# Kernel tuning notes

Measured on AMD Instinct MI355X. Metric: run time of the kernel, lower is better.

Reference implementation:

```python
import jax, jax.numpy as jnp
import numpy as np

VOCAB = 32000
DIM = 256
LAYERS = 2
CLASSES = 8
BATCH = 32
SEQ = 8192


def setup_inputs() -> dict:
    key = jax.random.key(0)
    ks = jax.random.split(key, 8)
    s = 1.0 / np.sqrt(DIM)
    x = jax.random.randint(ks[0], (BATCH, SEQ), 0, VOCAB, dtype=jnp.int32)
    emb = jax.random.normal(ks[1], (VOCAB, DIM), dtype=jnp.float32)
    Wz = jax.random.normal(ks[2], (LAYERS, DIM, DIM), dtype=jnp.float32) * s
    bz = jnp.zeros((LAYERS, DIM), dtype=jnp.float32)
    Wh = jax.random.normal(ks[3], (LAYERS, DIM, DIM), dtype=jnp.float32) * s
    bh = jnp.zeros((LAYERS, DIM), dtype=jnp.float32)
    Wo = jax.random.normal(ks[4], (DIM, CLASSES), dtype=jnp.float32) * s
    bo = jnp.zeros((CLASSES,), dtype=jnp.float32)
    return {"x": x, "emb": emb, "Wz": Wz, "bz": bz, "Wh": Wh, "bh": bh, "Wo": Wo, "bo": bo}


def _min_gru_layer(h_in, Wz_l, bz_l, Wh_l, bh_l):
    # minGRU: z_t = sigmoid(W_z x_t); h~_t = W_h x_t
    # h_t = (1 - z_t) * h_{t-1} + z_t * h~_t,  h_0 = 0
    z = jax.nn.sigmoid(jnp.einsum('bsd,de->bse', h_in, Wz_l) + bz_l)
    h_tilde = jnp.einsum('bsd,de->bse', h_in, Wh_l) + bh_l
    a = 1.0 - z          # decay coefficient
    b = z * h_tilde      # input contribution
    # parallel associative scan of h_t = a_t * h_{t-1} + b_t (h_0 = 0)
    def combine(c1, c2):
        a1, b1 = c1
        a2, b2 = c2
        return a1 * a2, b1 * a2 + b2
    _, h = jax.lax.associative_scan(combine, (a, b), axis=1)
    return h


def reference(x, emb, Wz, bz, Wh, bh, Wo, bo):
    h = emb[x]  # [B, S, D]
    for l in range(LAYERS):
        h = _min_gru_layer(h, Wz[l], bz[l], Wh[l], bh[l])
    # classifier on the last timestep
    return h[:, -1] @ Wo + bo  # [B, CLASSES]
```

## Files before the change

kernel.cpp:

```cpp
#include <hip/hip_runtime.h>
#include <stdint.h>

#define SEQ 8192
#define CS 64
#define NCH 128
#define NBLK 4096

typedef float f32x4 __attribute__((ext_vector_type(4)));
typedef short short8 __attribute__((ext_vector_type(8)));
typedef unsigned short u16;
typedef u16 ushort8 __attribute__((ext_vector_type(8)));
typedef u16 ushort4v __attribute__((ext_vector_type(4)));

__device__ __forceinline__ u16 f2bf(float f) {
  uint32_t u = __float_as_uint(f);
  u += 0x7fffu + ((u >> 16) & 1u);
  return (u16)(u >> 16);
}

__device__ __forceinline__ void gld16(void* lds, const void* g) {
  __builtin_amdgcn_global_load_lds(
      (const __attribute__((address_space(1))) uint32_t*)g,
      (__attribute__((address_space(3))) uint32_t*)lds, 16, 0, 0);
}

__global__ void embq_kernel(const float* __restrict__ emb, u16* __restrict__ embq) {
  int i = (blockIdx.x * 256 + threadIdx.x) * 4;
  float4 v = *(const float4*)(emb + i);
  ushort4v p;
  p[0] = f2bf(v.x); p[1] = f2bf(v.y); p[2] = f2bf(v.z); p[3] = f2bf(v.w);
  *(ushort4v*)(embq + i) = p;
}

__global__ void wt_kernel(const float* __restrict__ Wz, const float* __restrict__ Wh,
                          u16* __restrict__ WtS) {
  int idx = blockIdx.x * 256 + threadIdx.x;
  int d = idx & 255;
  int k = (idx >> 8) & 255;
  int m = idx >> 16;
  const float* src = (m < 2 ? Wz : Wh) + (size_t)(m & 1) * 65536;
  float v = src[k * 256 + d];
  int dh = d >> 6, dloc = d & 63, k32 = k >> 5, kl = k & 31;
  size_t tile = ((size_t)(m * 4 + dh) * 8 + k32) * 4096;
  size_t byte = (size_t)(dloc * 64 + ((kl * 2) ^ (((dloc >> 1) & 3) << 4)));
  *(u16*)((char*)WtS + tile + byte) = f2bf(v);
}

__device__ __forceinline__ void stage32(char* dst, const char* WtSb, int mat, int k32,
                                        int w, int lane) {
  const int dh = w >> 1, half = w & 1;
  const char* src = WtSb + ((size_t)((mat * 4 + dh) * 8 + k32)) * 4096 + half * 2048 + lane * 16;
  char* d = dst + dh * 4096 + half * 2048;
  gld16(d, src);
  gld16(d + 1024, src + 1024);
}

__device__ __forceinline__ void load_fa(const u16* As, int k32, int wr, int l15, int lg,
                                        short8 (&fa)[2]) {
  const int xm = (l15 & 7) << 4;
  const int kt = k32 >> 1, ks = k32 & 1;
  #pragma unroll
  for (int mi = 0; mi < 2; mi++)
    fa[mi] = *(const short8*)((const char*)As + kt * 8192 +
               (((wr * 32 + mi * 16 + l15) * 128 + ks * 64 + lg * 16) ^ xm));
}

__device__ __forceinline__ void mfma_frags(const char* P, const short8 (&fa)[2],
    int wc, int l15, int lg, f32x4 (&acc)[2][4])
{
  #pragma unroll
  for (int ni = 0; ni < 4; ni++) {
    const int dloc = ni * 16 + l15;
    const int off = dloc * 64 + ((lg * 16) ^ (((dloc >> 1) & 3) << 4));
    short8 fb = *(const short8*)(P + wc * 4096 + off);
    #pragma unroll
    for (int mi = 0; mi < 2; mi++)
      acc[mi][ni] = __builtin_amdgcn_mfma_f32_16x16x32_bf16(fa[mi], fb, acc[mi][ni], 0, 0, 0);
  }
}

__device__ __forceinline__ void gemm_pipe3(int lsel, const char* WtSb, const u16* As,
    char* Pb, int w, int wr, int wc, int l15, int lg, int lane,
    f32x4 (&accz)[2][4], f32x4 (&acch)[2][4])
{
  stage32(Pb,         WtSb, lsel,     0, w, lane);
  stage32(Pb + 16384, WtSb, 2 + lsel, 0, w, lane);
  short8 fa[2];
  #pragma unroll
  for (int i = 0; i < 16; ++i) {
    if (i < 15) asm volatile("s_waitcnt vmcnt(2)" ::: "memory");
    else        asm volatile("s_waitcnt vmcnt(0)" ::: "memory");
    __builtin_amdgcn_s_barrier();
    __builtin_amdgcn_sched_barrier(0);
    if (i + 2 < 16)
      stage32(Pb + ((i + 2) % 3) * 16384, WtSb,
              ((i + 2) & 1) ? (2 + lsel) : lsel, (i + 2) >> 1, w, lane);
    if ((i & 1) == 0) {
      load_fa(As, i >> 1, wr, l15, lg, fa);
      mfma_frags(Pb + (i % 3) * 16384, fa, wc, l15, lg, accz);
    } else {
      mfma_frags(Pb + (i % 3) * 16384, fa, wc, l15, lg, acch);
    }
  }
}

__device__ __forceinline__ float2* seg_ptr(char* segt, int s, int d) {
  return (float2*)(segt + s * 2048 + ((d * 8) ^ (s << 4)));
}

template<int PHASE>
__global__ __launch_bounds__(512, 4)
void gru_kernel(const int* __restrict__ x, const u16* __restrict__ embq,
                const u16* __restrict__ WtS,
                const float* __restrict__ bz0, const float* __restrict__ bh0,
                const float* __restrict__ bz1, const float* __restrict__ bh1,
                const float* __restrict__ carry,
                float* __restrict__ Ap, float* __restrict__ Bs)
{
  __shared__ __align__(16) u16 As[16384];
  __shared__ __align__(16) char Pb[49152];

  const int tid = threadIdx.x;
  const int lane = tid & 63;
  const int w = tid >> 6;
  const int wr = w >> 2, wc = w & 3;
  const int l15 = lane & 15, lg = lane >> 4;
  const int cb = blockIdx.x;
  const int b = cb >> 7, c = cb & (NCH - 1);
  const char* WtSb = (const char*)WtS;
  char* segt = (char*)As;

  {
    const int sm = tid >> 3, kq = tid & 7;
    const int tok = x[b * SEQ + c * CS + sm];
    const u16* src = embq + (size_t)tok * 256 + kq * 32;
    char* sub = (char*)As + (kq >> 1) * 8192;
    const int kb = (kq & 1) * 64;
    const int swz = (sm & 7) << 4;
    #pragma unroll
    for (int j = 0; j < 4; j++) {
      ushort8 p = *(const ushort8*)(src + j * 8);
      *(ushort8*)(sub + ((sm * 128 + kb + j * 16) ^ swz)) = p;
    }
  }

  f32x4 accz[2][4], acch[2][4];
  #pragma unroll
  for (int i = 0; i < 2; i++)
    #pragma unroll
    for (int j = 0; j < 4; j++) {
      f32x4 zz = {0.f, 0.f, 0.f, 0.f};
      accz[i][j] = zz; acch[i][j] = zz;
    }

  __syncthreads();
  gemm_pipe3(0, WtSb, As, Pb, w, wr, wc, l15, lg, lane, accz, acch);
  __syncthreads();

  #pragma unroll
  for (int ni = 0; ni < 4; ni++) {
    const int d = wc * 64 + ni * 16 + l15;
    const float bzv = bz0[d];
    const float bhv = bh0[d];
    #pragma unroll
    for (int mi = 0; mi < 2; mi++) {
      float A = 1.f, B = 0.f;
      #pragma unroll
      for (int r = 0; r < 4; r++) {
        float zl = accz[mi][ni][r] + bzv;
        float a = __builtin_amdgcn_rcpf(1.f + __expf(zl));
        float ht = acch[mi][ni][r] + bhv;
        float bb = (1.f - a) * ht;
        if (PHASE == 1) { accz[mi][ni][r] = a; acch[mi][ni][r] = bb; }
        B = B * a + bb;
        A *= a;
      }
      *seg_ptr(segt, wr * 8 + mi * 4 + lg, d) = make_float2(A, B);
    }
  }
  __syncthreads();

  if (PHASE == 0) {
    if (tid < 256) {
      float PA = 1.f, PB = 0.f;
      #pragma unroll
      for (int s = 0; s < 16; s++) {
        float2 v = *seg_ptr(segt, s, tid);
        PB = v.x * PB + v.y;
        PA *= v.x;
      }
      Ap[(size_t)cb * 256 + tid] = PA;
      Bs[(size_t)cb * 256 + tid] = PB;
    }
    return;
  }

  if (tid < 256) {
    float PA = 1.f, PB = 0.f;
    #pragma unroll
    for (int s = 0; s < 16; s++) {
      float2* p = seg_ptr(segt, s, tid);
      float2 v = *p;
      *p = make_float2(PA, PB);
      PB = v.x * PB + v.y;
      PA *= v.x;
    }
  }
  __syncthreads();

  float ea[2][4], eb[2][4], h0v[4];
  #pragma unroll
  for (int ni = 0; ni < 4; ni++) {
    const int d = wc * 64 + ni * 16 + l15;
    h0v[ni] = carry[(size_t)cb * 256 + d];
    #pragma unroll
    for (int mi = 0; mi < 2; mi++) {
      float2 e = *seg_ptr(segt, wr * 8 + mi * 4 + lg, d);
      ea[mi][ni] = e.x; eb[mi][ni] = e.y;
    }
  }
  __syncthreads();

  #pragma unroll
  for (int ni = 0; ni < 4; ni++) {
    const int d = wc * 64 + ni * 16 + l15;
    char* sub = (char*)As + (d >> 6) * 8192;
    const int kl2 = (d & 63) * 2;
    #pragma unroll
    for (int mi = 0; mi < 2; mi++) {
      float h = ea[mi][ni] * h0v[ni] + eb[mi][ni];
      #pragma unroll
      for (int r = 0; r < 4; r++) {
        h = accz[mi][ni][r] * h + acch[mi][ni][r];
        const int t = wr * 32 + mi * 16 + lg * 4 + r;
        *(u16*)(sub + ((t * 128 + kl2) ^ ((t & 7) << 4))) = f2bf(h);
      }
    }
  }

  #pragma unroll
  for (int i = 0; i < 2; i++)
    #pragma unroll
    for (int j = 0; j < 4; j++) {
      f32x4 zz = {0.f, 0.f, 0.f, 0.f};
      accz[i][j] = zz; acch[i][j] = zz;
    }

  __syncthreads();
  gemm_pipe3(1, WtSb, As, Pb, w, wr, wc, l15, lg, lane, accz, acch);
  __syncthreads();

  #pragma unroll
  for (int ni = 0; ni < 4; ni++) {
    const int d = wc * 64 + ni * 16 + l15;
    const float bzv = bz1[d];
    const float bhv = bh1[d];
    #pragma unroll
    for (int mi = 0; mi < 2; mi++) {
      float A = 1.f, B = 0.f;
      #pragma unroll
      for (int r = 0; r < 4; r++) {
        float zl = accz[mi][ni][r] + bzv;
        float a = __builtin_amdgcn_rcpf(1.f + __expf(zl));
        float ht = acch[mi][ni][r] + bhv;
        float bb = (1.f - a) * ht;
        B = B * a + bb;
        A *= a;
      }
      *seg_ptr(segt, wr * 8 + mi * 4 + lg, d) = make_float2(A, B);
    }
  }
  __syncthreads();
  if (tid < 256) {
    float PA = 1.f, PB = 0.f;
    #pragma unroll
    for (int s = 0; s < 16; s++) {
      float2 v = *seg_ptr(segt, s, tid);
      PB = v.x * PB + v.y;
      PA *= v.x;
    }
    Ap[(size_t)cb * 256 + tid] = PA;
    Bs[(size_t)cb * 256 + tid] = PB;
  }
}

__global__ void scan2_l0(const float* __restrict__ Ap0, const float* __restrict__ Bs0,
                         float* __restrict__ carry) {
  const int g = blockIdx.x * 256 + threadIdx.x;
  const int b = g >> 8, d = g & 255;
  float h = 0.f;
  for (int c = 0; c < NCH; c++) {
    const size_t idx = (size_t)(b * NCH + c) * 256 + d;
    carry[idx] = h;
    h = Bs0[idx] + Ap0[idx] * h;
  }
}

__global__ void scan2_l1(const float* __restrict__ Ap1, const float* __restrict__ Bs1,
                         float* __restrict__ hlast) {
  const int g = blockIdx.x * 256 + threadIdx.x;
  const int b = g >> 8, d = g & 255;
  float h = 0.f;
  for (int c = 0; c < NCH; c++) {
    const size_t idx = (size_t)(b * NCH + c) * 256 + d;
    h = Bs1[idx] + Ap1[idx] * h;
  }
  hlast[b * 256 + d] = h;
}

__global__ void cls_kernel(const float* __restrict__ hlast, const float* __restrict__ Wo,
                           const float* __restrict__ bo, float* __restrict__ out) {
  const int t = threadIdx.x;
  const int b = t >> 3, c = t & 7;
  float acc = bo[c];
  for (int d = 0; d < 256; d++) acc += hlast[b * 256 + d] * Wo[d * 8 + c];
  out[t] = acc;
}

extern "C" void kernel_launch(void* const* d_in, const int* in_sizes, int n_in,
                              void* d_out, int out_size, void* d_ws, size_t ws_size,
                              hipStream_t stream) {
  (void)in_sizes; (void)n_in; (void)out_size; (void)ws_size;
  const int*   x   = (const int*)d_in[0];
  const float* emb = (const float*)d_in[1];
  const float* Wz  = (const float*)d_in[2];
  const float* bz  = (const float*)d_in[3];
  const float* Wh  = (const float*)d_in[4];
  const float* bh  = (const float*)d_in[5];
  const float* Wo  = (const float*)d_in[6];
  const float* bo  = (const float*)d_in[7];
  float* out = (float*)d_out;
  char* ws = (char*)d_ws;

  u16*   embq  = (u16*)  (ws);
  u16*   WtS   = (u16*)  (ws + 16777216ull);
  float* Ap0   = (float*)(ws + 17301504ull);
  float* Bs0   = (float*)(ws + 21495808ull);
  float* carry = (float*)(ws + 25690112ull);
  float* Ap1   = (float*)(ws + 29884416ull);
  float* Bs1   = (float*)(ws + 34078720ull);
  float* hlast = (float*)(ws + 38273024ull);

  embq_kernel<<<8000, 256, 0, stream>>>(emb, embq);
  wt_kernel<<<1024, 256, 0, stream>>>(Wz, Wh, WtS);

  gru_kernel<0><<<NBLK, 512, 0, stream>>>(
      x, embq, WtS, bz, bh, bz + 256, bh + 256, nullptr, Ap0, Bs0);
  scan2_l0<<<32, 256, 0, stream>>>(Ap0, Bs0, carry);
  gru_kernel<1><<<NBLK, 512, 0, stream>>>(
      x, embq, WtS, bz, bh, bz + 256, bh + 256, carry, Ap1, Bs1);

  scan2_l1<<<32, 256, 0, stream>>>(Ap1, Bs1, hlast);
  cls_kernel<<<1, 256, 0, stream>>>(hlast, Wo, bo, out);
}
```

Before: 311.6 us.

## Use 4-wave blocks where each wave owns a 64-column weight slice, dropping per-stage barriers

Result: faster. 291.7 us (median of 2 runs) (-6.4%).

```diff
diff --git a/kernel.cpp b/kernel.cpp
--- a/kernel.cpp
+++ b/kernel.cpp
@@ -46,60 +46,58 @@
   *(u16*)((char*)WtS + tile + byte) = f2bf(v);
 }
 
-__device__ __forceinline__ void stage32(char* dst, const char* WtSb, int mat, int k32,
+__device__ __forceinline__ void stage32(char* dst_wave, const char* WtSb, int mat, int k32,
                                         int w, int lane) {
-  const int dh = w >> 1, half = w & 1;
-  const char* src = WtSb + ((size_t)((mat * 4 + dh) * 8 + k32)) * 4096 + half * 2048 + lane * 16;
-  char* d = dst + dh * 4096 + half * 2048;
-  gld16(d, src);
-  gld16(d + 1024, src + 1024);
-}
-
-__device__ __forceinline__ void load_fa(const u16* As, int k32, int wr, int l15, int lg,
-                                        short8 (&fa)[2]) {
+  const char* src = WtSb + ((size_t)((mat * 4 + w) * 8 + k32)) * 4096 + lane * 16;
+  #pragma unroll
+  for (int i = 0; i < 4; i++)
+    gld16(dst_wave + i * 1024, src + i * 1024);
+}
+
+__device__ __forceinline__ void load_fa(const u16* As, int k32, int l15, int lg,
+                                        short8 (&fa)[4]) {
   const int xm = (l15 & 7) << 4;
   const int kt = k32 >> 1, ks = k32 & 1;
   #pragma unroll
-  for (int mi = 0; mi < 2; mi++)
+  for (int mi = 0; mi < 4; mi++)
     fa[mi] = *(const short8*)((const char*)As + kt * 8192 +
-               (((wr * 32 + mi * 16 + l15) * 128 + ks * 64 + lg * 16) ^ xm));
-}
-
-__device__ __forceinline__ void mfma_frags(const char* P, const short8 (&fa)[2],
-    int wc, int l15, int lg, f32x4 (&acc)[2][4])
+               (((mi * 16 + l15) * 128 + ks * 64 + lg * 16) ^ xm));
+}
+
+__device__ __forceinline__ void mfma_frags(const char* Pw, const short8 (&fa)[4],
+    int l15, int lg, f32x4 (&acc)[4][4])
 {
   #pragma unroll
   for (int ni = 0; ni < 4; ni++) {
     const int dloc = ni * 16 + l15;
     const int off = dloc * 64 + ((lg * 16) ^ (((dloc >> 1) & 3) << 4));
-    short8 fb = *(const short8*)(P + wc * 4096 + off);
-    #pragma unroll
-    for (int mi = 0; mi < 2; mi++)
+    short8 fb = *(const short8*)(Pw + off);
+    #pragma unroll
+    for (int mi = 0; mi < 4; mi++)
       acc[mi][ni] = __builtin_amdgcn_mfma_f32_16x16x32_bf16(fa[mi], fb, acc[mi][ni], 0, 0, 0);
   }
 }
 
 __device__ __forceinline__ void gemm_pipe3(int lsel, const char* WtSb, const u16* As,
-    char* Pb, int w, int wr, int wc, int l15, int lg, int lane,
-    f32x4 (&accz)[2][4], f32x4 (&acch)[2][4])
+    char* Pw, int w, int l15, int lg, int lane,
+    f32x4 (&accz)[4][4], f32x4 (&acch)[4][4])
 {
-  stage32(Pb,         WtSb, lsel,     0, w, lane);
-  stage32(Pb + 16384, WtSb, 2 + lsel, 0, w, lane);
-  short8 fa[2];
+  stage32(Pw,         WtSb, lsel,     0, w, lane);
+  stage32(Pw + 16384, WtSb, 2 + lsel, 0, w, lane);
+  short8 fa[4];
   #pragma unroll
   for (int i = 0; i < 16; ++i) {
-    if (i < 15) asm volatile("s_waitcnt vmcnt(2)" ::: "memory");
+    if (i < 15) asm volatile("s_waitcnt vmcnt(4)" ::: "memory");
     else        asm volatile("s_waitcnt vmcnt(0)" ::: "memory");
-    __builtin_amdgcn_s_barrier();
     __builtin_amdgcn_sched_barrier(0);
     if (i + 2 < 16)
-      stage32(Pb + ((i + 2) % 3) * 16384, WtSb,
+      stage32(Pw + ((i + 2) % 3) * 16384, WtSb,
               ((i + 2) & 1) ? (2 + lsel) : lsel, (i + 2) >> 1, w, lane);
     if ((i & 1) == 0) {
-      load_fa(As, i >> 1, wr, l15, lg, fa);
-      mfma_frags(Pb + (i % 3) * 16384, fa, wc, l15, lg, accz);
+      load_fa(As, i >> 1, l15, lg, fa);
+      mfma_frags(Pw + (i % 3) * 16384, fa, l15, lg, accz);
     } else {
-      mfma_frags(Pb + (i % 3) * 16384, fa, wc, l15, lg, acch);
+      mfma_frags(Pw + (i % 3) * 16384, fa, l15, lg, acch);
     }
   }
 }
@@ -109,7 +107,7 @@
 }
 
 template<int PHASE>
-__global__ __launch_bounds__(512, 4)
+__global__ __launch_bounds__(256, 2)
 void gru_kernel(const int* __restrict__ x, const u16* __restrict__ embq,
                 const u16* __restrict__ WtS,
                 const float* __restrict__ bz0, const float* __restrict__ bh0,
@@ -123,30 +121,29 @@
   const int tid = threadIdx.x;
   const int lane = tid & 63;
   const int w = tid >> 6;
-  const int wr = w >> 2, wc = w & 3;
   const int l15 = lane & 15, lg = lane >> 4;
   const int cb = blockIdx.x;
   const int b = cb >> 7, c = cb & (NCH - 1);
   const char* WtSb = (const char*)WtS;
   char* segt = (char*)As;
+  char* Pw = Pb + w * 4096;
 
   {
-    const int sm = tid >> 3, kq = tid & 7;
+    const int sm = tid >> 2, kq = tid & 3;
     const int tok = x[b * SEQ + c * CS + sm];
-    const u16* src = embq + (size_t)tok * 256 + kq * 32;
-    char* sub = (char*)As + (kq >> 1) * 8192;
-    const int kb = (kq & 1) * 64;
+    const u16* src = embq + (size_t)tok * 256 + kq * 64;
+    char* sub = (char*)As + kq * 8192;
     const int swz = (sm & 7) << 4;
     #pragma unroll
-    for (int j = 0; j < 4; j++) {
+    for (int j = 0; j < 8; j++) {
       ushort8 p = *(const ushort8*)(src + j * 8);
-      *(ushort8*)(sub + ((sm * 128 + kb + j * 16) ^ swz)) = p;
-    }
-  }
-
-  f32x4 accz[2][4], acch[2][4];
-  #pragma unroll
-  for (int i = 0; i < 2; i++)
+      *(ushort8*)(sub + ((sm * 128 + j * 16) ^ swz)) = p;
+    }
+  }
+
+  f32x4 accz[4][4], acch[4][4];
+  #pragma unroll
+  for (int i = 0; i < 4; i++)
     #pragma unroll
     for (int j = 0; j < 4; j++) {
       f32x4 zz = {0.f, 0.f, 0.f, 0.f};
@@ -154,16 +151,16 @@
     }
 
   __syncthreads();
-  gemm_pipe3(0, WtSb, As, Pb, w, wr, wc, l15, lg, lane, accz, acch);
-  __syncthreads();
-
-  #pragma unroll
-  for (int ni = 0; ni < 4; ni++) {
-    const int d = wc * 64 + ni * 16 + l15;
+  gemm_pipe3(0, WtSb, As, Pw, w, l15, lg, lane, accz, acch);
+  __syncthreads();
+
+  #pragma unroll
+  for (int ni = 0; ni < 4; ni++) {
+    const int d = w * 64 + ni * 16 + l15;
     const float bzv = bz0[d];
     const float bhv = bh0[d];
     #pragma unroll
-    for (int mi = 0; mi < 2; mi++) {
+    for (int mi = 0; mi < 4; mi++) {
       float A = 1.f, B = 0.f;
       #pragma unroll
       for (int r = 0; r < 4; r++) {
@@ -175,27 +172,25 @@
         B = B * a + bb;
         A *= a;
       }
-      *seg_ptr(segt, wr * 8 + mi * 4 + lg, d) = make_float2(A, B);
+      *seg_ptr(segt, mi * 4 + lg, d) = make_float2(A, B);
     }
   }
   __syncthreads();
 
   if (PHASE == 0) {
-    if (tid < 256) {
-      float PA = 1.f, PB = 0.f;
-      #pragma unroll
-      for (int s = 0; s < 16; s++) {
-        float2 v = *seg_ptr(segt, s, tid);
-        PB = v.x * PB + v.y;
-        PA *= v.x;
-      }
-      Ap[(size_t)cb * 256 + tid] = PA;
-      Bs[(size_t)cb * 256 + tid] = PB;
-    }
+    float PA = 1.f, PB = 0.f;
+    #pragma unroll
+    for (int s = 0; s < 16; s++) {
+      float2 v = *seg_ptr(segt, s, tid);
+      PB = v.x * PB + v.y;
+      PA *= v.x;
+    }
+    Ap[(size_t)cb * 256 + tid] = PA;
+    Bs[(size_t)cb * 256 + tid] = PB;
     return;
   }
 
-  if (tid < 256) {
+  {
     float PA = 1.f, PB = 0.f;
     #pragma unroll
     for (int s = 0; s < 16; s++) {
@@ -208,14 +203,14 @@
   }
   __syncthreads();
 
-  float ea[2][4], eb[2][4], h0v[4];
-  #pragma unroll
-  for (int ni = 0; ni < 4; ni++) {
-    const int d = wc * 64 + ni * 16 + l15;
+  float ea[4][4], eb[4][4], h0v[4];
+  #pragma unroll
+  for (int ni = 0; ni < 4; ni++) {
+    const int d = w * 64 + ni * 16 + l15;
     h0v[ni] = carry[(size_t)cb * 256 + d];
     #pragma unroll
-    for (int mi = 0; mi < 2; mi++) {
-      float2 e = *seg_ptr(segt, wr * 8 + mi * 4 + lg, d);
+    for (int mi = 0; mi < 4; mi++) {
+      float2 e = *seg_ptr(segt, mi * 4 + lg, d);
       ea[mi][ni] = e.x; eb[mi][ni] = e.y;
     }
   }
@@ -223,23 +218,23 @@
 
   #pragma unroll
   for (int ni = 0; ni < 4; ni++) {
-    const int d = wc * 64 + ni * 16 + l15;
+    const int d = w * 64 + ni * 16 + l15;
     char* sub = (char*)As + (d >> 6) * 8192;
     const int kl2 = (d & 63) * 2;
     #pragma unroll
-    for (int mi = 0; mi < 2; mi++) {
+    for (int mi = 0; mi < 4; mi++) {
       float h = ea[mi][ni] * h0v[ni] + eb[mi][ni];
       #pragma unroll
       for (int r = 0; r < 4; r++) {
         h = accz[mi][ni][r] * h + acch[mi][ni][r];
-        const int t = wr * 32 + mi * 16 + lg * 4 + r;
+        const int t = mi * 16 + lg * 4 + r;
         *(u16*)(sub + ((t * 128 + kl2) ^ ((t & 7) << 4))) = f2bf(h);
       }
     }
   }
 
   #pragma unroll
-  for (int i = 0; i < 2; i++)
+  for (int i = 0; i < 4; i++)
     #pragma unroll
     for (int j = 0; j < 4; j++) {
       f32x4 zz = {0.f, 0.f, 0.f, 0.f};
@@ -247,16 +242,16 @@
     }
 
   __syncthreads();
-  gemm_pipe3(1, WtSb, As, Pb, w, wr, wc, l15, lg, lane, accz, acch);
-  __syncthreads();
-
-  #pragma unroll
-  for (int ni = 0; ni < 4; ni++) {
-    const int d = wc * 64 + ni * 16 + l15;
+  gemm_pipe3(1, WtSb, As, Pw, w, l15, lg, lane, accz, acch);
+  __syncthreads();
+
+  #pragma unroll
+  for (int ni = 0; ni < 4; ni++) {
+    const int d = w * 64 + ni * 16 + l15;
     const float bzv = bz1[d];
     const float bhv = bh1[d];
     #pragma unroll
-    for (int mi = 0; mi < 2; mi++) {
+    for (int mi = 0; mi < 4; mi++) {
       float A = 1.f, B = 0.f;
       #pragma unroll
       for (int r = 0; r < 4; r++) {
@@ -267,11 +262,11 @@
         B = B * a + bb;
         A *= a;
       }
-      *seg_ptr(segt, wr * 8 + mi * 4 + lg, d) = make_float2(A, B);
-    }
-  }
-  __syncthreads();
-  if (tid < 256) {
+      *seg_ptr(segt, mi * 4 + lg, d) = make_float2(A, B);
+    }
+  }
+  __syncthreads();
+  {
     float PA = 1.f, PB = 0.f;
     #pragma unroll
     for (int s = 0; s < 16; s++) {
@@ -344,10 +339,10 @@
   embq_kernel<<<8000, 256, 0, stream>>>(emb, embq);
   wt_kernel<<<1024, 256, 0, stream>>>(Wz, Wh, WtS);
 
-  gru_kernel<0><<<NBLK, 512, 0, stream>>>(
+  gru_kernel<0><<<NBLK, 256, 0, stream>>>(
       x, embq, WtS, bz, bh, bz + 256, bh + 256, nullptr, Ap0, Bs0);
   scan2_l0<<<32, 256, 0, stream>>>(Ap0, Bs0, carry);
-  gru_kernel<1><<<NBLK, 512, 0, stream>>>(
+  gru_kernel<1><<<NBLK, 256, 0, stream>>>(
       x, embq, WtS, bz, bh, bz + 256, bh + 256, carry, Ap1, Bs1);
 
   scan2_l1<<<32, 256, 0, stream>>>(Ap1, Bs1, hlast);
```
